# Kernel optimization log

Hardware: AMD Instinct MI355X
Metric: run time of the kernel (lower is better)

The kernel has to match this reference:

```python
import jax, jax.numpy as jnp
import numpy as np

BINS = 100
LOSS_WEIGHT = 1.0


def setup_inputs() -> dict:
    key = jax.random.key(0)
    k1, k2 = jax.random.split(key)
    B, C, H, W = 8, 19, 512, 512
    pred = jax.random.normal(k1, (B, C, H, W), dtype=jnp.float32)
    target = jax.random.randint(k2, (B, H, W), 0, C, dtype=jnp.int64)
    label_weight = jnp.ones((B, H, W), dtype=bool)
    return {"pred": pred, "target": target, "label_weight": label_weight}


def _ghmc(pred, target, label_weight):
    C = pred.shape[1]
    # _expand_onehot_labels: zero-out ignored labels, one-hot, expand mask
    tgt = jnp.where(label_weight, target, 0)
    t = jax.nn.one_hot(tgt, C, dtype=jnp.float32)              # [B,H,W,C]
    lw = jnp.broadcast_to(label_weight[..., None], t.shape)     # [B,H,W,C] bool
    x = jnp.transpose(pred, (0, 2, 3, 1))                       # [B,H,W,C]

    # gradient norm g = |sigmoid(pred).detach() - target|
    g = jnp.abs(jax.nn.sigmoid(jax.lax.stop_gradient(x)) - t)

    valid = lw
    valid_f = valid.astype(jnp.float32)
    tot = jnp.maximum(valid_f.sum(), 1.0)

    # histogram over BINS equal-width bins on [0, 1] (edges[-1] += 1e-6 -> g==1 in last bin)
    bin_idx = jnp.clip(jnp.floor(g * BINS).astype(jnp.int32), 0, BINS - 1)
    counts = jnp.zeros((BINS,), jnp.float32).at[bin_idx.ravel()].add(valid_f.ravel())
    n = (counts > 0).sum().astype(jnp.float32)  # number of non-empty bins

    # inverse-frequency weights: tot / num_in_bin for valid elements, then / n
    w = jnp.where(valid, tot / jnp.maximum(counts[bin_idx], 1.0), 0.0)
    w = jnp.where(n > 0, w / n, w)
    w = jax.lax.stop_gradient(w)

    # weighted BCE-with-logits, reduction='sum', normalized by tot
    bce = jnp.maximum(x, 0.0) - x * t + jnp.log1p(jnp.exp(-jnp.abs(x)))
    return (bce * w).sum() / tot * LOSS_WEIGHT


def reference(pred, target, label_weight):
    return _ghmc(pred, target, label_weight)
```

## Files before the change

### kernel.cpp

```cpp
#include <hip/hip_runtime.h>

#define BINS 100
#define NCOPY 16
#define HSTRIDE 101

typedef unsigned long long u64;

static constexpr unsigned kQ = 8u * 65536u;

__global__ void ghmc_zero(u64* __restrict__ g) {
    const int i = threadIdx.x;
    if (i < 2 * BINS) g[i] = 0ull;
}

__global__ __launch_bounds__(256, 4) void ghmc_main(
        const float* __restrict__ pred,
        const int*   __restrict__ target,
        const int*   __restrict__ lw,
        u64*         __restrict__ gacc)
{
    __shared__ u64 hist[NCOPY * HSTRIDE];

    const unsigned q    = blockIdx.x * 256u + threadIdx.x;
    const unsigned b    = q >> 16;
    const unsigned hw4  = q & 65535u;
    const unsigned base = ((b * 19u) << 16) | hw4;

    const int4 tg = reinterpret_cast<const int4*>(target)[q];
    const int4 lv = reinterpret_cast<const int4*>(lw)[q];
    float4 pv[19];
#pragma unroll
    for (int c = 0; c < 19; ++c)
        pv[c] = reinterpret_cast<const float4*>(pred)[base + ((unsigned)c << 16)];
    __builtin_amdgcn_sched_barrier(0);

    for (int i = threadIdx.x; i < NCOPY * HSTRIDE; i += 256) hist[i] = 0ull;
    __syncthreads();

    const int lane = threadIdx.x & 63;
    const int copy = ((threadIdx.x >> 6) << 2) | (lane & 3);
    u64* __restrict__ h = &hist[copy * HSTRIDE];

    const int ts[4] = {tg.x, tg.y, tg.z, tg.w};
    const int ls[4] = {lv.x, lv.y, lv.z, lv.w};

#pragma unroll
    for (int c = 0; c < 19; ++c) {
        const float xs[4] = {pv[c].x, pv[c].y, pv[c].z, pv[c].w};
#pragma unroll
        for (int j = 0; j < 4; ++j) {
            if (ls[j] == 0) continue;
            const float x   = xs[j];
            const bool  hit = (ts[j] == c);
            const bool  pos = hit ? (x <= 0.0f) : (x >= 0.0f);
            const float u   = __expf(-fabsf(x));
            const float r   = __builtin_amdgcn_rcpf(1.0f + u);
            const float ur  = u * r;
            const float g   = pos ? r : ur;
            const float omg = pos ? ur : r;
            int bin = (int)(g * 100.0f);
            bin = bin > (BINS - 1) ? (BINS - 1) : bin;
            const float bf  = fmaf(__logf(omg), -16777216.0f, 0.5f);
            const u64 inc = (1ull << 48) | (u64)(unsigned)bf;
            atomicAdd(&h[bin], inc);
        }
    }
    __syncthreads();

    if (threadIdx.x < BINS) {
        u64 s = 0ull;
#pragma unroll
        for (int cp = 0; cp < NCOPY; ++cp) s += hist[cp * HSTRIDE + threadIdx.x];
        const u64 cnt = s >> 48;
        if (cnt) {
            atomicAdd(&gacc[threadIdx.x], cnt);
            atomicAdd(&gacc[BINS + threadIdx.x], s & 0xFFFFFFFFFFFFull);
        }
    }
}

__global__ __launch_bounds__(128) void ghmc_final(
        const u64* __restrict__ gacc, float* __restrict__ out)
{
    __shared__ double sterm[128];
    __shared__ int    sn[128];
    const int t = threadIdx.x;
    double term = 0.0; int nn = 0;
    if (t < BINS) {
        const u64 c = gacc[t];
        if (c) { term = (double)gacc[BINS + t] / (16777216.0 * (double)c); nn = 1; }
    }
    sterm[t] = term; sn[t] = nn;
    __syncthreads();
    for (int s = 64; s > 0; s >>= 1) {
        if (t < s) { sterm[t] += sterm[t + s]; sn[t] += sn[t + s]; }
        __syncthreads();
    }
    if (t == 0) {
        const double loss = (sn[0] > 0) ? sterm[0] / (double)sn[0] : 0.0;
        out[0] = (float)loss;
    }
}

extern "C" void kernel_launch(void* const* d_in, const int* in_sizes, int n_in,
                              void* d_out, int out_size, void* d_ws, size_t ws_size,
                              hipStream_t stream) {
    const float* pred   = (const float*)d_in[0];
    const int*   target = (const int*)d_in[1];
    const int*   lw     = (const int*)d_in[2];
    float*       out    = (float*)d_out;
    u64*         gacc   = (u64*)d_ws;

    ghmc_zero <<<1,        256, 0, stream>>>(gacc);
    ghmc_main <<<kQ / 256, 256, 0, stream>>>(pred, target, lw, gacc);
    ghmc_final<<<1,        128, 0, stream>>>(gacc, out);
}
```

Baseline: 260.2 us.

## Replace shared-memory atomic histogram with per-thread private u32 bins

Each thread now owns a private column of a 100x128 u32 shared histogram, so the 64-bit LDS atomics are replaced by plain read-modify-write adds with no contention. Count and fixed-point log sum are packed into one u32 (7-bit count, 25-bit sum at 2^16 scale), which lowers precision versus the previous 24-bit fraction. Blocks shrink to 128 threads, and the final per-bin reduction walks 128 columns with a rotated index to avoid bank conflicts. The 51 KB of LDS per block limits occupancy, and the packed fields could overflow if one thread's per-bin log sum grows large.

```diff
diff --git a/kernel.cpp b/kernel.cpp
--- a/kernel.cpp
+++ b/kernel.cpp
@@ -1,10 +1,9 @@
 #include <hip/hip_runtime.h>
 
 #define BINS 100
-#define NCOPY 16
-#define HSTRIDE 101
 
 typedef unsigned long long u64;
+typedef unsigned int u32;
 
 static constexpr unsigned kQ = 8u * 65536u;
 
@@ -13,15 +12,16 @@
     if (i < 2 * BINS) g[i] = 0ull;
 }
 
-__global__ __launch_bounds__(256, 4) void ghmc_main(
+__global__ __launch_bounds__(128) void ghmc_main(
         const float* __restrict__ pred,
         const int*   __restrict__ target,
         const int*   __restrict__ lw,
         u64*         __restrict__ gacc)
 {
-    __shared__ u64 hist[NCOPY * HSTRIDE];
+    __shared__ u32 hist[BINS][128];
 
-    const unsigned q    = blockIdx.x * 256u + threadIdx.x;
+    const unsigned t    = threadIdx.x;
+    const unsigned q    = blockIdx.x * 128u + t;
     const unsigned b    = q >> 16;
     const unsigned hw4  = q & 65535u;
     const unsigned base = ((b * 19u) << 16) | hw4;
@@ -34,12 +34,8 @@
         pv[c] = reinterpret_cast<const float4*>(pred)[base + ((unsigned)c << 16)];
     __builtin_amdgcn_sched_barrier(0);
 
-    for (int i = threadIdx.x; i < NCOPY * HSTRIDE; i += 256) hist[i] = 0ull;
+    for (int i = t; i < BINS * 128; i += 128) (&hist[0][0])[i] = 0u;
     __syncthreads();
-
-    const int lane = threadIdx.x & 63;
-    const int copy = ((threadIdx.x >> 6) << 2) | (lane & 3);
-    u64* __restrict__ h = &hist[copy * HSTRIDE];
 
     const int ts[4] = {tg.x, tg.y, tg.z, tg.w};
     const int ls[4] = {lv.x, lv.y, lv.z, lv.w};
@@ -60,21 +56,24 @@
             const float omg = pos ? ur : r;
             int bin = (int)(g * 100.0f);
             bin = bin > (BINS - 1) ? (BINS - 1) : bin;
-            const float bf  = fmaf(__logf(omg), -16777216.0f, 0.5f);
-            const u64 inc = (1ull << 48) | (u64)(unsigned)bf;
-            atomicAdd(&h[bin], inc);
+            const float bf  = fmaf(__logf(omg), -65536.0f, 0.5f);
+            const u32 inc = (1u << 25) | (u32)bf;
+            hist[bin][t] += inc;
         }
     }
     __syncthreads();
 
-    if (threadIdx.x < BINS) {
-        u64 s = 0ull;
-#pragma unroll
-        for (int cp = 0; cp < NCOPY; ++cp) s += hist[cp * HSTRIDE + threadIdx.x];
-        const u64 cnt = s >> 48;
+    if (t < BINS) {
+        u64 cnt = 0ull, sum = 0ull;
+#pragma unroll 4
+        for (int k = 0; k < 128; ++k) {
+            const u32 cell = hist[t][(t + k) & 127];
+            cnt += cell >> 25;
+            sum += cell & 0x1FFFFFFu;
+        }
         if (cnt) {
-            atomicAdd(&gacc[threadIdx.x], cnt);
-            atomicAdd(&gacc[BINS + threadIdx.x], s & 0xFFFFFFFFFFFFull);
+            atomicAdd(&gacc[t], cnt);
+            atomicAdd(&gacc[BINS + t], sum);
         }
     }
 }
@@ -88,7 +87,7 @@
     double term = 0.0; int nn = 0;
     if (t < BINS) {
         const u64 c = gacc[t];
-        if (c) { term = (double)gacc[BINS + t] / (16777216.0 * (double)c); nn = 1; }
+        if (c) { term = (double)gacc[BINS + t] / (65536.0 * (double)c); nn = 1; }
     }
     sterm[t] = term; sn[t] = nn;
     __syncthreads();
@@ -112,6 +111,6 @@
     u64*         gacc   = (u64*)d_ws;
 
     ghmc_zero <<<1,        256, 0, stream>>>(gacc);
-    ghmc_main <<<kQ / 256, 256, 0, stream>>>(pred, target, lw, gacc);
+    ghmc_main <<<kQ / 128, 128, 0, stream>>>(pred, target, lw, gacc);
     ghmc_final<<<1,        128, 0, stream>>>(gacc, out);
 }
```

New measurement: 338.6 us. 1.3x slower.
